# Optimization experiments

Hardware: AMD Instinct MI355X
Metric: run time of the kernel (lower is better)

## Reference

```python
import jax, jax.numpy as jnp
import numpy as np

N = 100_000      # nodes
E = 1_600_000    # edges (before self-loops)
F_IN = 128       # num_features
H = 128          # nhid
G = 512          # graphs in batch
C = 10           # num_classes
EPS = 1e-5       # BatchNorm eps


def setup_inputs() -> dict:
    key = jax.random.key(0)
    ks = jax.random.split(key, 24)
    x = jax.random.normal(ks[0], (N, F_IN), jnp.float32)
    edge_index = jax.random.randint(ks[1], (2, E), 0, N, dtype=jnp.int64)
    batch = jnp.sort(jax.random.randint(ks[2], (N,), 0, G, dtype=jnp.int64))

    def lin(k, fi, fo):
        return jax.random.normal(k, (fi, fo), jnp.float32) / np.sqrt(fi).astype(np.float32)

    inp = dict(x=x, edge_index=edge_index, batch=batch)
    inp.update(
        W1=lin(ks[3], F_IN, H), b1=jnp.zeros((H,), jnp.float32),
        g1=jnp.ones((H,), jnp.float32), be1=jnp.zeros((H,), jnp.float32),
        W2=lin(ks[4], H, H), b2=jnp.zeros((H,), jnp.float32),
        g2=jnp.ones((H,), jnp.float32), be2=jnp.zeros((H,), jnp.float32),
        W3=lin(ks[5], H, H), b3=jnp.zeros((H,), jnp.float32),
        g3=jnp.ones((H,), jnp.float32), be3=jnp.zeros((H,), jnp.float32),
        gp=jnp.ones((H,), jnp.float32), bep=jnp.zeros((H,), jnp.float32),
        lw1=lin(ks[6], H, H), lb1=jnp.zeros((H,), jnp.float32),
        lw2=lin(ks[7], H, C), lb2=jnp.zeros((C,), jnp.float32),
    )
    return inp


def _batchnorm(h, g, b):
    # training-mode BatchNorm1d: batch stats, biased variance
    m = h.mean(axis=0)
    v = h.var(axis=0)
    return g * (h - m) * jax.lax.rsqrt(v + EPS) + b


def _gcn(h, W, b, src, dst, norm, n):
    # GCNConv: h @ W, then normalized gather-scatter aggregation
    h = h @ W
    msg = h[src] * norm[:, None]                     # [E+N, H] gather
    out = jax.ops.segment_sum(msg, dst, num_segments=n)
    return out + b


def reference(x, edge_index, batch, W1, b1, g1, be1, W2, b2, g2, be2,
              W3, b3, g3, be3, gp, bep, lw1, lb1, lw2, lb2):
    n = x.shape[0]
    loops = jnp.arange(n, dtype=edge_index.dtype)
    src = jnp.concatenate([edge_index[0], loops])
    dst = jnp.concatenate([edge_index[1], loops])
    # symmetric normalization D^{-1/2} (A+I) D^{-1/2}
    deg = jax.ops.segment_sum(jnp.ones_like(src, dtype=x.dtype), dst, num_segments=n)
    dis = jnp.where(deg > 0, jax.lax.rsqrt(jnp.maximum(deg, 1.0)), 0.0)
    norm = dis[src] * dis[dst]

    h = jax.nn.relu(_batchnorm(_gcn(x, W1, b1, src, dst, norm, n), g1, be1))
    h = jax.nn.relu(_batchnorm(_gcn(h, W2, b2, src, dst, norm, n), g2, be2))
    h = jax.nn.relu(_batchnorm(_gcn(h, W3, b3, src, dst, norm, n), g3, be3))

    # global_mean_pool over graph ids
    counts = jax.ops.segment_sum(jnp.ones((n,), x.dtype), batch, num_segments=G)
    pooled = jax.ops.segment_sum(h, batch, num_segments=G) / jnp.maximum(counts, 1.0)[:, None]

    z = _batchnorm(pooled, gp, bep)
    z = jax.nn.relu(z @ lw1 + lb1)
    # dropout_ratio=0.0 -> identity
    z = z @ lw2 + lb2
    return jax.nn.log_softmax(z, axis=-1)
```

## Files before the change

### kernel.cpp

```cpp
#include <hip/hip_runtime.h>
#include <hip/hip_bf16.h>
#include <cstdint>

#define HDIM 128

typedef __bf16 bf16x8 __attribute__((ext_vector_type(8)));
typedef unsigned short usx8 __attribute__((ext_vector_type(8)));
typedef float fx4 __attribute__((ext_vector_type(4)));

__device__ __forceinline__ float bf2f(unsigned short u) {
    unsigned int x = ((unsigned int)u) << 16;
    return __uint_as_float(x);
}
__device__ __forceinline__ unsigned short f2bf(float f) {
    unsigned int x = __float_as_uint(f);
    x += 0x7fffu + ((x >> 16) & 1u);
    return (unsigned short)(x >> 16);
}

__device__ __forceinline__ void detect_local(const unsigned int* xw, const unsigned int* eiw,
                                             int& f0, int& f1) {
    int sane = 0;
    for (int k = 0; k < 64; k++) {
        unsigned int w = xw[k];
        unsigned short ss[2] = {(unsigned short)(w & 0xffffu), (unsigned short)(w >> 16)};
        for (int q = 0; q < 2; q++) {
            int e = (ss[q] >> 7) & 0xFF;
            if ((ss[q] & 0x7fffu) == 0 || (e >= 100 && e <= 140)) sane++;
        }
    }
    f0 = (sane >= 110) ? 1 : 0;
    int zeros = 0;
    for (int k = 1; k < 64; k += 2)
        if (eiw[k] == 0) zeros++;
    f1 = (zeros >= 24) ? 1 : 0;
}

struct ParamTab {
    const void* p[15];
    int n[15];
    int off[15];
};

__global__ void phase1(const unsigned int* __restrict__ xw, const unsigned int* __restrict__ eiw,
                       const void* __restrict__ ei, const void* __restrict__ batch,
                       const void* __restrict__ W1, const void* __restrict__ W2,
                       const void* __restrict__ W3, ParamTab tab, int* __restrict__ flags,
                       float* __restrict__ gsumAll, int* __restrict__ Ct,
                       unsigned short* __restrict__ wconv, unsigned short* __restrict__ Wf,
                       int* __restrict__ goff, int* __restrict__ gcnt, int E, int N, int G,
                       int NB, int ntiles, int TILE) {
    __shared__ int h[1024];
    __shared__ int lf0s, lf1s;
    int b = blockIdx.x, t = threadIdx.x;
    if (t == 0) {
        int a0, a1;
        detect_local(xw, eiw, a0, a1);
        lf0s = a0;
        lf1s = a1;
    }
    __syncthreads();
    int lf0 = lf0s, lf1 = lf1s;
    if (b < ntiles) {
        for (int i = t; i < NB; i += 256) h[i] = 0;
        __syncthreads();
        int base = b * TILE;
        for (int i = t; i < TILE; i += 256) {
            int idx = base + i;
            if (idx < E) {
                int d = lf1 ? (int)((const long long*)ei)[(size_t)E + idx]
                            : ((const int*)ei)[(size_t)E + idx];
                atomicAdd(&h[d >> 9], 1);
            }
        }
        __syncthreads();
        for (int k = t; k < NB; k += 256) Ct[k * ntiles + b] = h[k];
    } else if (b < ntiles + 15) {
        int pb = b - ntiles;
        const void* src = tab.p[pb];
        int n = tab.n[pb];
        unsigned short* o = wconv + tab.off[pb];
        if (lf0) {
            const unsigned short* s = (const unsigned short*)src;
            for (int i = t; i < n; i += 256) o[i] = s[i];
        } else {
            const float* s = (const float*)src;
            for (int i = t; i < n; i += 256) o[i] = f2bf(s[i]);
        }
    } else if (b < ntiles + 17) {
        int gi = (b - ntiles - 15) * 256 + t;
        if (gi < G) {
            auto getb = [&](int i) -> int {
                return lf1 ? (int)((const long long*)batch)[i] : ((const int*)batch)[i];
            };
            auto lower = [&](int val) -> int {
                int lo = 0, hi = N;
                while (lo < hi) {
                    int mid = (lo + hi) >> 1;
                    if (getb(mid) < val) lo = mid + 1;
                    else hi = mid;
                }
                return lo;
            };
            int lo = lower(gi), hi = lower(gi + 1);
            goff[gi] = lo;
            gcnt[gi] = hi - lo;
        }
    } else if (b < ntiles + 17 + 24) {
        int idx = (b - ntiles - 17) * 256 + t;
        int layer = idx >> 11;
        int rem = idx & 2047;
        int kt = rem >> 9;
        int nt = (rem >> 6) & 7;
        int lane = rem & 63;
        const void* W = (layer == 0) ? W1 : ((layer == 1) ? W2 : W3);
        int row = lane & 15, quad = lane >> 4;
        unsigned short* o = Wf + ((size_t)layer * 2048 + (size_t)((kt * 8 + nt) * 64 + lane)) * 8;
#pragma unroll
        for (int j = 0; j < 8; j++) {
            int k = kt * 32 + quad * 8 + j;
            int off = k * HDIM + nt * 16 + row;
            o[j] = lf0 ? ((const unsigned short*)W)[off] : f2bf(((const float*)W)[off]);
        }
    } else {
        for (int i = t; i < 12288; i += 256) gsumAll[i] = 0.f;
        if (t == 0) {
            flags[0] = lf0;
            flags[1] = lf1;
        }
    }
}

__global__ void s1_scan(int* __restrict__ Ct, int* __restrict__ btot, int NB, int ntiles) {
    __shared__ int buf[512];
    int b = blockIdx.x, t = threadIdx.x;
    int v = (t < ntiles) ? Ct[b * ntiles + t] : 0;
    buf[t] = v;
    __syncthreads();
    for (int o = 1; o < 512; o <<= 1) {
        int a = (t >= o) ? buf[t - o] : 0;
        __syncthreads();
        buf[t] += a;
        __syncthreads();
    }
    if (t < ntiles) Ct[b * ntiles + t] = buf[t] - v;
    if (t == 0) btot[b] = buf[511];
}

__global__ void p1_scatter(const void* __restrict__ ei, const int* __restrict__ flags,
                           const int* __restrict__ Ct, const int* __restrict__ btot,
                           unsigned int* __restrict__ pairs, int E, int NB, int ntiles,
                           int TILE) {
    __shared__ int cur[1024];
    __shared__ int bb[256];
    int tile = blockIdx.x, t = threadIdx.x;
    int v = (t < NB) ? btot[t] : 0;
    bb[t] = v;
    __syncthreads();
    for (int o = 1; o < 256; o <<= 1) {
        int a = (t >= o) ? bb[t - o] : 0;
        __syncthreads();
        bb[t] += a;
        __syncthreads();
    }
    if (t < NB) cur[t] = (bb[t] - v) + Ct[t * ntiles + tile];
    __syncthreads();
    int base = tile * TILE;
    bool i64 = flags[1] != 0;
    for (int i = t; i < TILE; i += 256) {
        int idx = base + i;
        if (idx < E) {
            int s, d;
            if (i64) {
                s = (int)((const long long*)ei)[idx];
                d = (int)((const long long*)ei)[(size_t)E + idx];
            } else {
                s = ((const int*)ei)[idx];
                d = ((const int*)ei)[(size_t)E + idx];
            }
            int pos = atomicAdd(&cur[d >> 9], 1);
            pairs[pos] = ((unsigned)(d & 511) << 23) | (unsigned)s;
        }
    }
}

__global__ void p2_build(const unsigned int* __restrict__ pairs, const int* __restrict__ btot,
                         int* __restrict__ csrc, int* __restrict__ offs, int* __restrict__ cnt,
                         float* __restrict__ dis, int E, int N, int NB) {
    __shared__ int hist[512];
    __shared__ int start[512];
    __shared__ int cur[512];
    __shared__ int ps[256];
    __shared__ int bb[256];
    __shared__ int sh_excl[256];
    int b = blockIdx.x, t = threadIdx.x;
    int node0 = b * 512;
    int v = (t < NB) ? btot[t] : 0;
    bb[t] = v;
    __syncthreads();
    for (int o = 1; o < 256; o <<= 1) {
        int a = (t >= o) ? bb[t - o] : 0;
        __syncthreads();
        bb[t] += a;
        __syncthreads();
    }
    sh_excl[t] = bb[t] - v;
    for (int i = t; i < 512; i += 256) hist[i] = 0;
    __syncthreads();
    int lo = sh_excl[b];
    int hi = lo + ((b < NB) ? btot[b] : 0);
    for (int i = lo + t; i < hi; i += 256) {
        atomicAdd(&hist[pairs[i] >> 23], 1);
    }
    __syncthreads();
    ps[t] = hist[2 * t] + hist[2 * t + 1];
    __syncthreads();
    for (int o = 1; o < 256; o <<= 1) {
        int a = (t >= o) ? ps[t - o] : 0;
        __syncthreads();
        ps[t] += a;
        __syncthreads();
    }
    int e = t ? ps[t - 1] : 0;
    start[2 * t] = e;
    start[2 * t + 1] = e + hist[2 * t];
    __syncthreads();
    for (int i = t; i < 512; i += 256) {
        cur[i] = 0;
        int node = node0 + i;
        if (node < N) {
            offs[node] = lo + start[i];
            cnt[node] = hist[i];
            dis[node] = rsqrtf((float)(hist[i] + 1));
        }
    }
    __syncthreads();
    for (int i = lo + t; i < hi; i += 256) {
        unsigned int p = pairs[i];
        int l = p >> 23;
        int pos = lo + start[l] + atomicAdd(&cur[l], 1);
        csrc[pos] = (int)(p & 0x7fffffu);
    }
}

__global__ __launch_bounds__(256) void mm_mfma(const void* __restrict__ A,
                                               const unsigned short* __restrict__ Wf,
                                               unsigned short* __restrict__ C, int M,
                                               const float* __restrict__ gsumPrev,
                                               const unsigned short* __restrict__ gamma,
                                               const unsigned short* __restrict__ beta,
                                               const float* __restrict__ dis,
                                               const int* __restrict__ flags, int l0mode,
                                               float invn) {
    __shared__ float scs[128], shs[128];
    __shared__ unsigned short ldsC[4 * 16 * 136];
    int t = threadIdx.x;
    if (!l0mode && t < 128) {
        float s = 0.f, s2 = 0.f;
#pragma unroll
        for (int r = 0; r < 16; r++) {
            s += gsumPrev[r * 256 + t];
            s2 += gsumPrev[r * 256 + 128 + t];
        }
        float m = s * invn;
        float vv = s2 * invn - m * m;
        float sc = bf2f(gamma[t]) * rsqrtf(vv + 1e-5f);
        scs[t] = sc;
        shs[t] = bf2f(beta[t]) - m * sc;
    }
    __syncthreads();
    int gid = blockIdx.x * blockDim.x + t;
    int wave = gid >> 6;
    int lane = t & 63;
    int wv = t >> 6;
    int m0 = wave * 16;
    if (m0 >= M) return;
    int row = lane & 15, quad = lane >> 4;
    bool xfp32 = l0mode && !flags[0];
    const unsigned short* arow = (const unsigned short*)A + (size_t)(m0 + row) * HDIM + quad * 8;
    const float* arowf = (const float*)A + (size_t)(m0 + row) * HDIM + quad * 8;
    fx4 acc[8];
#pragma unroll
    for (int k = 0; k < 8; k++) acc[k] = (fx4){0.f, 0.f, 0.f, 0.f};
#pragma unroll
    for (int kt = 0; kt < 4; kt++) {
        bf16x8 a;
        if (xfp32) {
            fx4 f0 = *(const fx4*)(arowf + kt * 32);
            fx4 f1 = *(const fx4*)(arowf + kt * 32 + 4);
            usx8 tt;
#pragma unroll
            for (int q = 0; q < 4; q++) tt[q] = f2bf(f0[q]);
#pragma unroll
            for (int q = 0; q < 4; q++) tt[4 + q] = f2bf(f1[q]);
            a = __builtin_bit_cast(bf16x8, tt);
        } else {
            usx8 raw = *(const usx8*)(arow + kt * 32);
            if (!l0mode) {
                int col = kt * 32 + quad * 8;
                fx4 s0 = *(const fx4*)&scs[col];
                fx4 s1 = *(const fx4*)&scs[col + 4];
                fx4 h0 = *(const fx4*)&shs[col];
                fx4 h1 = *(const fx4*)&shs[col + 4];
                usx8 tt;
#pragma unroll
                for (int q = 0; q < 4; q++)
                    tt[q] = f2bf(fmaxf(s0[q] * bf2f(raw[q]) + h0[q], 0.f));
#pragma unroll
                for (int q = 0; q < 4; q++)
                    tt[4 + q] = f2bf(fmaxf(s1[q] * bf2f(raw[4 + q]) + h1[q], 0.f));
                a = __builtin_bit_cast(bf16x8, tt);
            } else {
                a = __builtin_bit_cast(bf16x8, raw);
            }
        }
        const unsigned short* wf = Wf + ((size_t)(kt * 8) * 64 + lane) * 8;
#pragma unroll
        for (int nt = 0; nt < 8; nt++) {
            bf16x8 bfr = __builtin_bit_cast(bf16x8, *(const usx8*)(wf + (size_t)nt * 64 * 8));
            acc[nt] = __builtin_amdgcn_mfma_f32_16x16x32_bf16(a, bfr, acc[nt], 0, 0, 0);
        }
    }
    float dsc[4];
#pragma unroll
    for (int r = 0; r < 4; r++) dsc[r] = dis[m0 + quad * 4 + r];
    unsigned short* lw = ldsC + wv * 16 * 136;
#pragma unroll
    for (int nt = 0; nt < 8; nt++) {
        int col = nt * 16 + row;
#pragma unroll
        for (int r = 0; r < 4; r++) {
            lw[(quad * 4 + r) * 136 + col] = f2bf(acc[nt][r] * dsc[r]);
        }
    }
    int row16 = lane >> 2;
    int seg = lane & 3;
    const unsigned short* src = lw + row16 * 136 + seg * 32;
    unsigned short* dst = C + (size_t)(m0 + row16) * HDIM + seg * 32;
#pragma unroll
    for (int k = 0; k < 4; k++) {
        *(usx8*)(dst + k * 8) = *(const usx8*)(src + k * 8);
    }
}

__global__ __launch_bounds__(256, 8) void aggregate(const unsigned short* __restrict__ hw,
                                                    const float* __restrict__ dis,
                                                    const int* __restrict__ offs,
                                                    const int* __restrict__ cnt,
                                                    const int* __restrict__ csrc,
                                                    const unsigned short* __restrict__ bias,
                                                    unsigned short* __restrict__ agg,
                                                    float* __restrict__ gsum16, int n) {
    __shared__ float red[16 * 128];
    int t = threadIdx.x;
    int lane = t & 63;
    int wv = t >> 6;
    int grp = lane >> 4, sub = lane & 15;
    int colb = sub * 8;
    usx8 bv = *(const usx8*)(bias + colb);
    float csum[8], csq[8];
#pragma unroll
    for (int q = 0; q < 8; q++) {
        csum[q] = 0.f;
        csq[q] = 0.f;
    }
    int stride = gridDim.x * 16;
    for (int node = blockIdx.x * 16 + wv * 4 + grp; node < n; node += stride) {
        usx8 sv = *(const usx8*)(hw + (size_t)node * HDIM + colb);
        float a[8];
#pragma unroll
        for (int q = 0; q < 8; q++) a[q] = bf2f(sv[q]);
        int o = offs[node], c = cnt[node];
        int s0 = (c > 0) ? csrc[o] : 0;
        int s1 = (c > 1) ? csrc[o + 1] : 0;
        int s2 = (c > 2) ? csrc[o + 2] : 0;
        int s3 = (c > 3) ? csrc[o + 3] : 0;
        int j = 0;
        while (j < c) {
            usx8 v0 = *(const usx8*)(hw + (size_t)s0 * HDIM + colb);
            usx8 v1 = *(const usx8*)(hw + (size_t)s1 * HDIM + colb);
            usx8 v2 = *(const usx8*)(hw + (size_t)s2 * HDIM + colb);
            usx8 v3 = *(const usx8*)(hw + (size_t)s3 * HDIM + colb);
            s0 = (j + 4 < c) ? csrc[o + j + 4] : 0;
            s1 = (j + 5 < c) ? csrc[o + j + 5] : 0;
            s2 = (j + 6 < c) ? csrc[o + j + 6] : 0;
            s3 = (j + 7 < c) ? csrc[o + j + 7] : 0;
#pragma unroll
            for (int q = 0; q < 8; q++) a[q] += bf2f(v0[q]);
            if (j + 1 < c) {
#pragma unroll
                for (int q = 0; q < 8; q++) a[q] += bf2f(v1[q]);
            }
            if (j + 2 < c) {
#pragma unroll
                for (int q = 0; q < 8; q++) a[q] += bf2f(v2[q]);
            }
            if (j + 3 < c) {
#pragma unroll
                for (int q = 0; q < 8; q++) a[q] += bf2f(v3[q]);
            }
            j += 4;
        }
        float di = dis[node];
        usx8 ov;
#pragma unroll
        for (int q = 0; q < 8; q++) {
            float val = bf2f(bv[q]) + di * a[q];
            ov[q] = f2bf(val);
            float vr = bf2f(ov[q]);
            csum[q] += vr;
            csq[q] += vr * vr;
        }
        *(usx8*)(agg + (size_t)node * HDIM + colb) = ov;
    }
    int gidx = wv * 4 + grp;
    int rep = (blockIdx.x & 15) * 256;
#pragma unroll
    for (int q = 0; q < 8; q++) red[gidx * 128 + colb + q] = csum[q];
    __syncthreads();
    if (t < 128) {
        float s = 0.f;
#pragma unroll
        for (int g = 0; g < 16; g++) s += red[g * 128 + t];
        atomicAdd(&gsum16[rep + t], s);
    }
    __syncthreads();
#pragma unroll
    for (int q = 0; q < 8; q++) red[gidx * 128 + colb + q] = csq[q];
    __syncthreads();
    if (t < 128) {
        float s = 0.f;
#pragma unroll
        for (int g = 0; g < 16; g++) s += red[g * 128 + t];
        atomicAdd(&gsum16[rep + 128 + t], s);
    }
}

__global__ void pool(const unsigned short* __restrict__ hin, const int* __restrict__ goff,
                     const int* __restrict__ gcnt, const float* __restrict__ gsum3,
                     const unsigned short* __restrict__ gamma,
                     const unsigned short* __restrict__ beta, float* __restrict__ pooled,
                     float invn) {
    __shared__ float scs[128], shs[128];
    __shared__ float ls[256];
    int g = blockIdx.x, t = threadIdx.x;
    if (t < 128) {
        float s = 0.f, s2 = 0.f;
#pragma unroll
        for (int r = 0; r < 16; r++) {
            s += gsum3[r * 256 + t];
            s2 += gsum3[r * 256 + 128 + t];
        }
        float m = s * invn;
        float vv = s2 * invn - m * m;
        float sc = bf2f(gamma[t]) * rsqrtf(vv + 1e-5f);
        scs[t] = sc;
        shs[t] = bf2f(beta[t]) - m * sc;
    }
    __syncthreads();
    int c = t & 127, p = t >> 7;
    float scale = scs[c], shift = shs[c];
    int s = goff[g], cn = gcnt[g];
    float acc = 0.f;
    for (int r = s + p; r < s + cn; r += 2)
        acc += fmaxf(scale * bf2f(hin[(size_t)r * HDIM + c]) + shift, 0.f);
    ls[t] = acc;
    __syncthreads();
    if (t < 128) pooled[(size_t)g * HDIM + t] = (ls[t] + ls[t + 128]) / fmaxf((float)cn, 1.f);
}
__global__ void pooled_bn(const float* __restrict__ pooled, const unsigned short* __restrict__ g,
                          const unsigned short* __restrict__ be, float* __restrict__ psc,
                          float* __restrict__ psh, int G_) {
    int t = threadIdx.x;
    int c = t & 127, p = t >> 7;
    float s = 0.f, s2 = 0.f;
    for (int r = p; r < G_; r += 4) {
        float v = pooled[(size_t)r * HDIM + c];
        s += v;
        s2 += v * v;
    }
    __shared__ float ls[512], ls2[512];
    ls[t] = s;
    ls2[t] = s2;
    __syncthreads();
    if (t < 128) {
        float S = ls[t] + ls[t + 128] + ls[t + 256] + ls[t + 384];
        float S2 = ls2[t] + ls2[t + 128] + ls2[t + 256] + ls2[t + 384];
        float m = S / (float)G_;
        float v = S2 / (float)G_ - m * m;
        float sc = bf2f(g[t]) * rsqrtf(v + 1e-5f);
        psc[t] = sc;
        psh[t] = bf2f(be[t]) - m * sc;
    }
}
__global__ void mlp12(const float* __restrict__ pooled, const float* __restrict__ psc,
                      const float* __restrict__ psh, const unsigned short* __restrict__ lw1,
                      const unsigned short* __restrict__ lb1,
                      const unsigned short* __restrict__ lw2,
                      const unsigned short* __restrict__ lb2, void* __restrict__ out,
                      const int* __restrict__ flags) {
    int r = blockIdx.x, t = threadIdx.x;
    __shared__ float row[128];
    __shared__ float z1s[128];
    __shared__ float z2[10];
    __shared__ float lse;
    row[t] = psc[t] * pooled[(size_t)r * HDIM + t] + psh[t];
    __syncthreads();
    float acc = bf2f(lb1[t]);
    for (int k = 0; k < 128; k++) acc += row[k] * bf2f(lw1[k * HDIM + t]);
    z1s[t] = fmaxf(acc, 0.f);
    __syncthreads();
    if (t < 10) {
        float a = bf2f(lb2[t]);
        for (int k = 0; k < 128; k++) a += z1s[k] * bf2f(lw2[k * 10 + t]);
        z2[t] = a;
    }
    __syncthreads();
    if (t == 0) {
        float m = z2[0];
        for (int j = 1; j < 10; j++) m = fmaxf(m, z2[j]);
        float s = 0.f;
        for (int j = 0; j < 10; j++) s += expf(z2[j] - m);
        lse = m + logf(s);
    }
    __syncthreads();
    if (t < 10) {
        float v = z2[t] - lse;
        if (flags[0]) ((unsigned short*)out)[r * 10 + t] = f2bf(v);
        else ((float*)out)[r * 10 + t] = v;
    }
}

extern "C" void kernel_launch(void* const* d_in, const int* in_sizes, int n_in,
                              void* d_out, int out_size, void* d_ws, size_t ws_size,
                              hipStream_t stream) {
    const void* x = d_in[0];
    const void* ei = d_in[1];
    const void* batch = d_in[2];

    int N_ = in_sizes[2];
    int E_ = in_sizes[1] / 2;
    int G_ = out_size / 10;

    const int TILE = 4096;
    int NB = (N_ + 511) / 512;
    int ntiles = (E_ + TILE - 1) / TILE;
    int L = NB * ntiles;

    char* ws = (char*)d_ws;
    auto alloc = [&](size_t bytes) -> char* {
        char* p = ws;
        ws += (bytes + 255) & ~(size_t)255;
        return p;
    };
    int* flags = (int*)alloc(256);
    float* dis = (float*)alloc((size_t)N_ * 4);
    int* offs = (int*)alloc((size_t)N_ * 4);
    int* cnt = (int*)alloc((size_t)N_ * 4);
    int* Ct = (int*)alloc((size_t)L * 4);
    int* btot = (int*)alloc(1024);
    unsigned int* pairs = (unsigned int*)alloc((size_t)E_ * 4);
    int* csrc = (int*)alloc((size_t)E_ * 4);
    unsigned short* hw = (unsigned short*)alloc((size_t)N_ * HDIM * 2);
    unsigned short* aggbuf = (unsigned short*)alloc((size_t)N_ * HDIM * 2);
    unsigned short* wconv = (unsigned short*)alloc(70000 * 2);
    unsigned short* wfrag = (unsigned short*)alloc(3 * HDIM * HDIM * 2);
    float* gsumAll = (float*)alloc(12288 * 4);
    int* gcnt = (int*)alloc((size_t)G_ * 4);
    int* goff = (int*)alloc((size_t)G_ * 4);
    float* pooled = (float*)alloc((size_t)G_ * HDIM * 4);
    float* psc = (float*)alloc(128 * 4);
    float* psh = (float*)alloc(128 * 4);

    const int oB = 49152;
    const int oLB1 = oB + 1408;
    const int oLW1 = oLB1 + 128;
    const int oLW2 = oLW1 + 16384;
    const int oLB2 = oLW2 + 1280;

    ParamTab tab;
    const int srcIdx[15] = {4, 5, 6, 8, 9, 10, 12, 13, 14, 15, 16, 18, 17, 19, 20};
    const int dstOff[15] = {oB + 0, oB + 128, oB + 256,
                            oB + 384, oB + 512, oB + 640,
                            oB + 768, oB + 896, oB + 1024,
                            oB + 1152, oB + 1280,
                            oLB1, oLW1, oLW2, oLB2};
    for (int i = 0; i < 15; i++) {
        tab.p[i] = d_in[srcIdx[i]];
        tab.n[i] = in_sizes[srcIdx[i]];
        tab.off[i] = dstOff[i];
    }

    int p1_grid = ntiles + 15 + 2 + 24 + 1;
    phase1<<<p1_grid, 256, 0, stream>>>((const unsigned int*)x, (const unsigned int*)ei, ei,
                                        batch, d_in[3], d_in[7], d_in[11], tab, flags, gsumAll,
                                        Ct, wconv, wfrag, goff, gcnt, E_, N_, G_, NB, ntiles,
                                        TILE);
    s1_scan<<<NB, 512, 0, stream>>>(Ct, btot, NB, ntiles);
    p1_scatter<<<ntiles, 256, 0, stream>>>(ei, flags, Ct, btot, pairs, E_, NB, ntiles, TILE);
    p2_build<<<NB, 256, 0, stream>>>(pairs, btot, csrc, offs, cnt, dis, E_, N_, NB);

    int mm_blocks = (((N_ + 15) / 16) * 64 + 255) / 256;
    float invn = 1.f / (float)N_;

    for (int l = 0; l < 3; l++) {
        const void* A = (l == 0) ? x : (const void*)aggbuf;
        const float* gp = (l == 0) ? nullptr : (gsumAll + (size_t)(l - 1) * 4096);
        const unsigned short* gam = wconv + oB + (l ? (l - 1) * 384 + 128 : 0);
        const unsigned short* bet = wconv + oB + (l ? (l - 1) * 384 + 256 : 0);
        mm_mfma<<<mm_blocks, 256, 0, stream>>>(A, wfrag + (size_t)l * HDIM * HDIM, hw, N_, gp,
                                               gam, bet, dis, flags, (l == 0) ? 1 : 0, invn);
        aggregate<<<2048, 256, 0, stream>>>(hw, dis, offs, cnt, csrc, wconv + oB + l * 384,
                                            aggbuf, gsumAll + (size_t)l * 4096, N_);
    }

    pool<<<G_, 256, 0, stream>>>(aggbuf, goff, gcnt, gsumAll + 2 * 4096,
                                 wconv + oB + 2 * 384 + 128, wconv + oB + 2 * 384 + 256, pooled,
                                 invn);
    pooled_bn<<<1, 512, 0, stream>>>(pooled, wconv + oB + 1152, wconv + oB + 1280, psc, psh, G_);
    mlp12<<<G_, 128, 0, stream>>>(pooled, psc, psh, wconv + oLW1, wconv + oLB1, wconv + oLW2,
                                  wconv + oLB2, d_out, flags);
}
```

Baseline: 545.7 us.

## Store node features in column-block-major layout so aggregation gathers from per-slice arrays

```diff
diff --git a/kernel.cpp b/kernel.cpp
--- a/kernel.cpp
+++ b/kernel.cpp
@@ -279,6 +279,7 @@
     bool xfp32 = l0mode && !flags[0];
     const unsigned short* arow = (const unsigned short*)A + (size_t)(m0 + row) * HDIM + quad * 8;
     const float* arowf = (const float*)A + (size_t)(m0 + row) * HDIM + quad * 8;
+    const unsigned short* ablk = (const unsigned short*)A;
     fx4 acc[8];
 #pragma unroll
     for (int k = 0; k < 8; k++) acc[k] = (fx4){0.f, 0.f, 0.f, 0.f};
@@ -294,25 +295,25 @@
 #pragma unroll
             for (int q = 0; q < 4; q++) tt[4 + q] = f2bf(f1[q]);
             a = __builtin_bit_cast(bf16x8, tt);
+        } else if (l0mode) {
+            usx8 raw = *(const usx8*)(arow + kt * 32);
+            a = __builtin_bit_cast(bf16x8, raw);
         } else {
-            usx8 raw = *(const usx8*)(arow + kt * 32);
-            if (!l0mode) {
-                int col = kt * 32 + quad * 8;
-                fx4 s0 = *(const fx4*)&scs[col];
-                fx4 s1 = *(const fx4*)&scs[col + 4];
-                fx4 h0 = *(const fx4*)&shs[col];
-                fx4 h1 = *(const fx4*)&shs[col + 4];
-                usx8 tt;
-#pragma unroll
-                for (int q = 0; q < 4; q++)
-                    tt[q] = f2bf(fmaxf(s0[q] * bf2f(raw[q]) + h0[q], 0.f));
-#pragma unroll
-                for (int q = 0; q < 4; q++)
-                    tt[4 + q] = f2bf(fmaxf(s1[q] * bf2f(raw[4 + q]) + h1[q], 0.f));
-                a = __builtin_bit_cast(bf16x8, tt);
-            } else {
-                a = __builtin_bit_cast(bf16x8, raw);
-            }
+            int c0 = kt * 32 + quad * 8;
+            usx8 raw =
+                *(const usx8*)(ablk + ((size_t)(c0 >> 4) * M + (m0 + row)) * 16 + (c0 & 15));
+            fx4 s0 = *(const fx4*)&scs[c0];
+            fx4 s1 = *(const fx4*)&scs[c0 + 4];
+            fx4 h0 = *(const fx4*)&shs[c0];
+            fx4 h1 = *(const fx4*)&shs[c0 + 4];
+            usx8 tt;
+#pragma unroll
+            for (int q = 0; q < 4; q++)
+                tt[q] = f2bf(fmaxf(s0[q] * bf2f(raw[q]) + h0[q], 0.f));
+#pragma unroll
+            for (int q = 0; q < 4; q++)
+                tt[4 + q] = f2bf(fmaxf(s1[q] * bf2f(raw[4 + q]) + h1[q], 0.f));
+            a = __builtin_bit_cast(bf16x8, tt);
         }
         const unsigned short* wf = Wf + ((size_t)(kt * 8) * 64 + lane) * 8;
 #pragma unroll
@@ -333,106 +334,122 @@
             lw[(quad * 4 + r) * 136 + col] = f2bf(acc[nt][r] * dsc[r]);
         }
     }
-    int row16 = lane >> 2;
-    int seg = lane & 3;
-    const unsigned short* src = lw + row16 * 136 + seg * 32;
-    unsigned short* dst = C + (size_t)(m0 + row16) * HDIM + seg * 32;
+    int sub8 = lane & 7, cbw = lane >> 3;
 #pragma unroll
     for (int k = 0; k < 4; k++) {
-        *(usx8*)(dst + k * 8) = *(const usx8*)(src + k * 8);
-    }
-}
-
-__global__ __launch_bounds__(256, 8) void aggregate(const unsigned short* __restrict__ hw,
-                                                    const float* __restrict__ dis,
-                                                    const int* __restrict__ offs,
-                                                    const int* __restrict__ cnt,
-                                                    const int* __restrict__ csrc,
-                                                    const unsigned short* __restrict__ bias,
-                                                    unsigned short* __restrict__ agg,
-                                                    float* __restrict__ gsum16, int n) {
-    __shared__ float red[16 * 128];
+        int ci = k * 8 + sub8;
+        int nd = ci >> 1, half = ci & 1;
+        if (m0 + nd < M) {
+            const unsigned short* src = lw + nd * 136 + cbw * 16 + half * 8;
+            unsigned short* dst = C + ((size_t)cbw * M + (m0 + nd)) * 16 + half * 8;
+            *(usx8*)dst = *(const usx8*)src;
+        }
+    }
+}
+
+__global__ void aggregate(const unsigned short* __restrict__ hw, const float* __restrict__ dis,
+                          const int* __restrict__ offs, const int* __restrict__ cnt,
+                          const int* __restrict__ csrc, const unsigned short* __restrict__ bias,
+                          unsigned short* __restrict__ agg, float* __restrict__ gsum16, int n) {
+    __shared__ float red[256 * 8];
     int t = threadIdx.x;
     int lane = t & 63;
     int wv = t >> 6;
-    int grp = lane >> 4, sub = lane & 15;
-    int colb = sub * 8;
-    usx8 bv = *(const usx8*)(bias + colb);
+    int cb = blockIdx.x & 7;
+    int gidx = blockIdx.x >> 3;
+    int P = gridDim.x >> 3;
+    int colOff = (lane & 1) * 8;
+    usx8 bv = *(const usx8*)(bias + cb * 16 + colOff);
+    const unsigned short* hslice = hw + (size_t)cb * n * 16;
+    unsigned short* aslice = agg + (size_t)cb * n * 16;
     float csum[8], csq[8];
 #pragma unroll
     for (int q = 0; q < 8; q++) {
         csum[q] = 0.f;
         csq[q] = 0.f;
     }
-    int stride = gridDim.x * 16;
-    for (int node = blockIdx.x * 16 + wv * 4 + grp; node < n; node += stride) {
-        usx8 sv = *(const usx8*)(hw + (size_t)node * HDIM + colb);
-        float a[8];
-#pragma unroll
-        for (int q = 0; q < 8; q++) a[q] = bf2f(sv[q]);
-        int o = offs[node], c = cnt[node];
-        int s0 = (c > 0) ? csrc[o] : 0;
-        int s1 = (c > 1) ? csrc[o + 1] : 0;
-        int s2 = (c > 2) ? csrc[o + 2] : 0;
-        int s3 = (c > 3) ? csrc[o + 3] : 0;
-        int j = 0;
-        while (j < c) {
-            usx8 v0 = *(const usx8*)(hw + (size_t)s0 * HDIM + colb);
-            usx8 v1 = *(const usx8*)(hw + (size_t)s1 * HDIM + colb);
-            usx8 v2 = *(const usx8*)(hw + (size_t)s2 * HDIM + colb);
-            usx8 v3 = *(const usx8*)(hw + (size_t)s3 * HDIM + colb);
-            s0 = (j + 4 < c) ? csrc[o + j + 4] : 0;
-            s1 = (j + 5 < c) ? csrc[o + j + 5] : 0;
-            s2 = (j + 6 < c) ? csrc[o + j + 6] : 0;
-            s3 = (j + 7 < c) ? csrc[o + j + 7] : 0;
-#pragma unroll
-            for (int q = 0; q < 8; q++) a[q] += bf2f(v0[q]);
-            if (j + 1 < c) {
-#pragma unroll
-                for (int q = 0; q < 8; q++) a[q] += bf2f(v1[q]);
+    for (int node0 = gidx * 128; node0 < n; node0 += P * 128) {
+        int node = node0 + wv * 32 + (lane >> 1);
+        if (node < n) {
+            usx8 sv = *(const usx8*)(hslice + (size_t)node * 16 + colOff);
+            float a[8];
+#pragma unroll
+            for (int q = 0; q < 8; q++) a[q] = bf2f(sv[q]);
+            int o = offs[node], c = cnt[node];
+            int s0 = (c > 0) ? csrc[o] : 0;
+            int s1 = (c > 1) ? csrc[o + 1] : 0;
+            int s2 = (c > 2) ? csrc[o + 2] : 0;
+            int s3 = (c > 3) ? csrc[o + 3] : 0;
+            int j = 0;
+            while (j < c) {
+                usx8 v0 = *(const usx8*)(hslice + (size_t)s0 * 16 + colOff);
+                usx8 v1 = *(const usx8*)(hslice + (size_t)s1 * 16 + colOff);
+                usx8 v2 = *(const usx8*)(hslice + (size_t)s2 * 16 + colOff);
+                usx8 v3 = *(const usx8*)(hslice + (size_t)s3 * 16 + colOff);
+                s0 = (j + 4 < c) ? csrc[o + j + 4] : 0;
+                s1 = (j + 5 < c) ? csrc[o + j + 5] : 0;
+                s2 = (j + 6 < c) ? csrc[o + j + 6] : 0;
+                s3 = (j + 7 < c) ? csrc[o + j + 7] : 0;
+#pragma unroll
+                for (int q = 0; q < 8; q++) a[q] += bf2f(v0[q]);
+                if (j + 1 < c) {
+#pragma unroll
+                    for (int q = 0; q < 8; q++) a[q] += bf2f(v1[q]);
+                }
+                if (j + 2 < c) {
+#pragma unroll
+                    for (int q = 0; q < 8; q++) a[q] += bf2f(v2[q]);
+                }
+                if (j + 3 < c) {
+#pragma unroll
+                    for (int q = 0; q < 8; q++) a[q] += bf2f(v3[q]);
+                }
+                j += 4;
             }
-            if (j + 2 < c) {
-#pragma unroll
-                for (int q = 0; q < 8; q++) a[q] += bf2f(v2[q]);
+            float di = dis[node];
+            usx8 ov;
+#pragma unroll
+            for (int q = 0; q < 8; q++) {
+                float val = bf2f(bv[q]) + di * a[q];
+                ov[q] = f2bf(val);
+                float vr = bf2f(ov[q]);
+                csum[q] += vr;
+                csq[q] += vr * vr;
             }
-            if (j + 3 < c) {
-#pragma unroll
-                for (int q = 0; q < 8; q++) a[q] += bf2f(v3[q]);
-            }
-            j += 4;
-        }
-        float di = dis[node];
-        usx8 ov;
-#pragma unroll
-        for (int q = 0; q < 8; q++) {
-            float val = bf2f(bv[q]) + di * a[q];
-            ov[q] = f2bf(val);
-            float vr = bf2f(ov[q]);
-            csum[q] += vr;
-            csq[q] += vr * vr;
-        }
-        *(usx8*)(agg + (size_t)node * HDIM + colb) = ov;
-    }
-    int gidx = wv * 4 + grp;
-    int rep = (blockIdx.x & 15) * 256;
-#pragma unroll
-    for (int q = 0; q < 8; q++) red[gidx * 128 + colb + q] = csum[q];
-    __syncthreads();
-    if (t < 128) {
-        float s = 0.f;
-#pragma unroll
-        for (int g = 0; g < 16; g++) s += red[g * 128 + t];
-        atomicAdd(&gsum16[rep + t], s);
-    }
-    __syncthreads();
-#pragma unroll
-    for (int q = 0; q < 8; q++) red[gidx * 128 + colb + q] = csq[q];
-    __syncthreads();
-    if (t < 128) {
-        float s = 0.f;
-#pragma unroll
-        for (int g = 0; g < 16; g++) s += red[g * 128 + t];
-        atomicAdd(&gsum16[rep + 128 + t], s);
+            __builtin_nontemporal_store(ov, (usx8*)(aslice + (size_t)node * 16 + colOff));
+        }
+    }
+    int rep = (gidx & 15) * 256;
+#pragma unroll
+    for (int q = 0; q < 8; q++) red[t * 8 + q] = csum[q];
+    __syncthreads();
+    for (int s = 128; s >= 2; s >>= 1) {
+        if (t < s) {
+#pragma unroll
+            for (int q = 0; q < 8; q++) red[t * 8 + q] += red[(t + s) * 8 + q];
+        }
+        __syncthreads();
+    }
+    if (t < 2) {
+#pragma unroll
+        for (int q = 0; q < 8; q++)
+            atomicAdd(&gsum16[rep + cb * 16 + t * 8 + q], red[t * 8 + q]);
+    }
+    __syncthreads();
+#pragma unroll
+    for (int q = 0; q < 8; q++) red[t * 8 + q] = csq[q];
+    __syncthreads();
+    for (int s = 128; s >= 2; s >>= 1) {
+        if (t < s) {
+#pragma unroll
+            for (int q = 0; q < 8; q++) red[t * 8 + q] += red[(t + s) * 8 + q];
+        }
+        __syncthreads();
+    }
+    if (t < 2) {
+#pragma unroll
+        for (int q = 0; q < 8; q++)
+            atomicAdd(&gsum16[rep + 128 + cb * 16 + t * 8 + q], red[t * 8 + q]);
     }
 }
 
@@ -440,7 +457,7 @@
                      const int* __restrict__ gcnt, const float* __restrict__ gsum3,
                      const unsigned short* __restrict__ gamma,
                      const unsigned short* __restrict__ beta, float* __restrict__ pooled,
-                     float invn) {
+                     float invn, int N_) {
     __shared__ float scs[128], shs[128];
     __shared__ float ls[256];
     int g = blockIdx.x, t = threadIdx.x;
@@ -461,9 +478,10 @@
     int c = t & 127, p = t >> 7;
     float scale = scs[c], shift = shs[c];
     int s = goff[g], cn = gcnt[g];
+    const unsigned short* base = hin + (size_t)(c >> 4) * N_ * 16 + (c & 15);
     float acc = 0.f;
     for (int r = s + p; r < s + cn; r += 2)
-        acc += fmaxf(scale * bf2f(hin[(size_t)r * HDIM + c]) + shift, 0.f);
+        acc += fmaxf(scale * bf2f(base[(size_t)r * 16]) + shift, 0.f);
     ls[t] = acc;
     __syncthreads();
     if (t < 128) pooled[(size_t)g * HDIM + t] = (ls[t] + ls[t + 128]) / fmaxf((float)cn, 1.f);
@@ -616,7 +634,7 @@
 
     pool<<<G_, 256, 0, stream>>>(aggbuf, goff, gcnt, gsumAll + 2 * 4096,
                                  wconv + oB + 2 * 384 + 128, wconv + oB + 2 * 384 + 256, pooled,
-                                 invn);
+                                 invn, N_);
     pooled_bn<<<1, 512, 0, stream>>>(pooled, wconv + oB + 1152, wconv + oB + 1280, psc, psh, G_);
     mlp12<<<G_, 128, 0, stream>>>(pooled, psc, psh, wconv + oLW1, wconv + oLB1, wconv + oLW2,
                                   wconv + oLB2, d_out, flags);
```

Measured after the change: 604.1 us. 1.11x slower.
